# Kernel optimization log

Measured on AMD Instinct MI355X. Metric: run time of the kernel, lower is better.

The kernel has to match this reference:

```python
import jax, jax.numpy as jnp
import numpy as np

NUM_HEADS = 12


def setup_inputs() -> dict:
    key = jax.random.key(0)
    k1, k2, k3 = jax.random.split(key, 3)
    B, N, C = 2, 2048, 768
    x = jax.random.normal(k1, (B, N, C), dtype=jnp.float32)
    # torch nn.Linear weights: [out_features, in_features]
    w_qkv = jax.random.normal(k2, (3 * C, C), dtype=jnp.float32) * (C ** -0.5)
    w_mlp = jax.random.normal(k3, (C, C), dtype=jnp.float32) * (C ** -0.5)
    b_mlp = jnp.zeros((C,), dtype=jnp.float32)
    return {"x": x, "w_qkv": w_qkv, "w_mlp": w_mlp, "b_mlp": b_mlp}


def reference(x, w_qkv, w_mlp, b_mlp):
    B, N, C = x.shape
    H = NUM_HEADS
    hd = C // H
    scale = hd ** -0.5
    # qkv linear (no bias), then the module's reshape: [B,N,H,3,hd]
    qkv = (x @ w_qkv.T).reshape(B, N, H, 3, hd)
    # permute(3,0,2,1,4) -> q,k,v each [B,H,N,hd]
    q = jnp.transpose(qkv[:, :, :, 0, :], (0, 2, 1, 3))
    k = jnp.transpose(qkv[:, :, :, 1, :], (0, 2, 1, 3))
    v = jnp.transpose(qkv[:, :, :, 2, :], (0, 2, 1, 3))
    attn = jax.nn.softmax(jnp.einsum('bhqd,bhkd->bhqk', q, k) * scale, axis=-1)
    out = jnp.einsum('bhqk,bhkd->bhqd', attn, v)          # [B,H,N,hd]
    out = jnp.transpose(out, (0, 2, 1, 3)).reshape(B, N, C)
    return out @ w_mlp.T + b_mlp
```

## Files before the change

kernel.cpp:

```cpp
#include <hip/hip_runtime.h>
#include <math.h>

typedef unsigned short u16;
typedef unsigned int   u32;
typedef __attribute__((ext_vector_type(8))) short s8v;
typedef __attribute__((ext_vector_type(2))) unsigned int u32x2;
typedef __attribute__((ext_vector_type(4))) float f4v;

#define NHEADS 12
#define SEQ 2048
#define CD 768
#define BB 2
#define QKVD 2304
#define CEXP 0.18033688f
#define DEFER_THR 44.0f

__device__ inline u16 f2bf(float f) {
    union { float f; unsigned u; } v; v.f = f;
    unsigned r = v.u + 0x7FFFu + ((v.u >> 16) & 1u);
    return (u16)(r >> 16);
}
__device__ inline u32 cvtpk_bf16(float lo, float hi) {
    u32 r;
    asm("v_cvt_pk_bf16_f32 %0, %1, %2" : "=v"(r) : "v"(lo), "v"(hi));
    return r;
}
__device__ inline float exp2_fast(float x) {
    float r;
    asm("v_exp_f32 %0, %1" : "=v"(r) : "v"(x));
    return r;
}
__device__ inline float max3f(float a, float b, float c) {
    float r;
    asm("v_max3_f32 %0, %1, %2, %3" : "=v"(r) : "v"(a), "v"(b), "v"(c));
    return r;
}

#define GLOAD16(SRC, DST) __builtin_amdgcn_global_load_lds(                 \
    (const __attribute__((address_space(1))) void*)(SRC),                   \
    (__attribute__((address_space(3))) void*)(DST), 16, 0, 0)

#define SW(r, c) ((((r) << 6) + (c)) ^ (((r) & 7) << 3))

__global__ __launch_bounds__(256)
void cvt3_kernel(const float* __restrict__ a, u16* __restrict__ oa, int na,
                 const float* __restrict__ b, u16* __restrict__ ob, int nb,
                 const float* __restrict__ c, u16* __restrict__ oc) {
    const int i = (blockIdx.x * 256 + threadIdx.x) * 8;
    const float* src; u16* dst;
    if (i < na)           { src = a + i;            dst = oa + i; }
    else if (i < na + nb) { src = b + (i - na);     dst = ob + (i - na); }
    else                  { src = c + (i - na - nb); dst = oc + (i - na - nb); }
    const float4 x = *(const float4*)src;
    const float4 y = *(const float4*)(src + 4);
    s8v o;
    o[0] = (short)f2bf(x.x); o[1] = (short)f2bf(x.y);
    o[2] = (short)f2bf(x.z); o[3] = (short)f2bf(x.w);
    o[4] = (short)f2bf(y.x); o[5] = (short)f2bf(y.y);
    o[6] = (short)f2bf(y.z); o[7] = (short)f2bf(y.w);
    *(s8v*)dst = o;
}

template<int BN, int NBX, bool OUT_BF16, bool BIAS>
__global__ __launch_bounds__(256)
void gemm_bf16(const u16* __restrict__ A, const u16* __restrict__ W,
               const float* __restrict__ bias, void* __restrict__ Cout,
               int M, int N, int K) {
    constexpr int NF = BN / 32;
    __shared__ u16 As[8192];
    __shared__ u16 Bs[BN * 64];
    const int tid = threadIdx.x;
    const int l  = tid & 63, w = tid >> 6;
    const int wr = w >> 1, wc = w & 1;
    const int lq = l & 15, lg = l >> 4;

    const int fid = blockIdx.x;
    const int cpx = gridDim.x >> 3;
    const int swz = (fid & 7) * cpx + (fid >> 3);
    const int rowBase = (swz / NBX) << 7;
    const int colBase = (swz % NBX) * BN;

    f4v acc[4][NF];
    #pragma unroll
    for (int m = 0; m < 4; ++m)
        #pragma unroll
        for (int n = 0; n < NF; ++n)
            #pragma unroll
            for (int r = 0; r < 4; ++r) acc[m][n][r] = 0.f;

    const int chunk = l & 7;
    const int r8    = l >> 3;

    for (int kb = 0; kb < K; kb += 64) {
        __syncthreads();
        #pragma unroll
        for (int j = 0; j < 4; ++j) {
            const int rowA = (w << 5) + (j << 3) + r8;
            const int sc   = (chunk ^ (rowA & 7)) << 3;
            GLOAD16(A + (size_t)(rowBase + rowA) * K + kb + sc,
                    &As[(w << 11) + (j << 9)]);
        }
        #pragma unroll
        for (int j = 0; j < NF; ++j) {
            const int rowB = w * (BN / 4) + (j << 3) + r8;
            const int sc   = (chunk ^ (rowB & 7)) << 3;
            GLOAD16(W + (size_t)(colBase + rowB) * K + kb + sc,
                    &Bs[w * (BN * 16) + (j << 9)]);
        }
        __syncthreads();
        #pragma unroll
        for (int h = 0; h < 2; ++h) {
            const int kc = (h << 5) + (lg << 3);
            s8v af[4], bf[NF];
            #pragma unroll
            for (int m = 0; m < 4; ++m)
                af[m] = *(const s8v*)&As[SW((wr << 6) + (m << 4) + lq, kc)];
            #pragma unroll
            for (int n = 0; n < NF; ++n)
                bf[n] = *(const s8v*)&Bs[SW(wc * (BN / 2) + (n << 4) + lq, kc)];
            #pragma unroll
            for (int m = 0; m < 4; ++m)
                #pragma unroll
                for (int n = 0; n < NF; ++n)
                    acc[m][n] = __builtin_amdgcn_mfma_f32_16x16x32_bf16(
                        af[m], bf[n], acc[m][n], 0, 0, 0);
        }
    }

    #pragma unroll
    for (int m = 0; m < 4; ++m)
        #pragma unroll
        for (int r = 0; r < 4; ++r) {
            const int row = rowBase + (wr << 6) + (m << 4) + (lg << 2) + r;
            #pragma unroll
            for (int n = 0; n < NF; ++n) {
                const int col = colBase + wc * (BN / 2) + (n << 4) + lq;
                float v = acc[m][n][r];
                if (BIAS) v += bias[col];
                if (OUT_BF16) ((u16*)Cout)[(size_t)row * N + col] = f2bf(v);
                else        ((float*)Cout)[(size_t)row * N + col] = v;
            }
        }
}

__global__ __launch_bounds__(256)
void vtrans_kernel(const u16* __restrict__ qkvb, u16* __restrict__ vT) {
    __shared__ u16 T[64][66];
    const int bh = blockIdx.y;
    const int tt = blockIdx.x;
    const int b = bh / NHEADS, h = bh % NHEADS;
    const int r  = threadIdx.x >> 2;
    const int dc = (threadIdx.x & 3) << 4;
    const u16* src = qkvb + (size_t)(b * SEQ + tt * 64 + r) * QKVD
                   + h * 192 + 128 + dc;
    *(s8v*)&T[r][dc]     = *(const s8v*)(src);
    *(s8v*)&T[r][dc + 8] = *(const s8v*)(src + 8);
    __syncthreads();
    const int d  = threadIdx.x >> 2;
    const int tc = (threadIdx.x & 3) << 4;
    s8v o0, o1;
    #pragma unroll
    for (int j = 0; j < 8; ++j) {
        o0[j] = (short)T[tc + j][d];
        o1[j] = (short)T[tc + 8 + j][d];
    }
    u16* dst = vT + ((size_t)bh * 64 + d) * SEQ + tt * 64 + tc;
    *(s8v*)dst = o0;
    *(s8v*)(dst + 8) = o1;
}

__global__ __launch_bounds__(512)
void attn_mfma(const u16* __restrict__ qkv, const u16* __restrict__ vT,
               u16* __restrict__ outb) {
    __shared__ u16 SL[24576];
    const int tid = threadIdx.x;
    const int l = tid & 63, w = tid >> 6;
    const int g = w >> 2, wl = w & 3;
    const int lq = l & 15, lg = l >> 4;

    const int fid = blockIdx.x;
    const int swz = (fid & 7) * 96 + (fid >> 3);
    const int q0 = (swz & 31) << 6;
    const int bh = swz >> 5;
    const int b = bh / NHEADS, h = bh % NHEADS;
    const u16* base = qkv + (size_t)b * SEQ * QKVD + h * 192;
    const u16* vbh  = vT + (size_t)bh * 64 * SEQ;
    u16* QP = SL + 16384;
    float* Of32 = (float*)(SL + 8192);
    float* Msh  = (float*)(SL + 16384);
    float* Lsh  = Msh + 64;

    const int kv0 = g << 10;

    u32 koff[2], voff[2], kdst[2], vdst[2];
    {
        const int cs = l & 7;
        #pragma unroll
        for (int i = 0; i < 2; ++i) {
            const int row = (wl << 4) + (i << 3) + (l >> 3);
            koff[i] = (u32)(row * QKVD + 64 + ((cs ^ (row & 7)) << 3));
            voff[i] = (u32)(row * SEQ  +      ((cs ^ (row & 7)) << 3));
            kdst[i] = (u32)((g << 13) + (wl << 10) + (i << 9));
            vdst[i] = (u32)((g << 13) + 4096 + (wl << 10) + (i << 9));
        }
    }

    {
        const u16* sbK = base + (size_t)kv0 * QKVD;
        const u16* sbV = vbh + kv0;
        #pragma unroll
        for (int i = 0; i < 2; ++i) {
            GLOAD16(sbK + koff[i], &SL[kdst[i]]);
            GLOAD16(sbV + voff[i], &SL[vdst[i]]);
        }
    }
    {
        const s8v q1 = *(const s8v*)(base + (size_t)(q0 + l) * QKVD + (w << 3));
        *(s8v*)&QP[SW(l, w << 3)] = q1;
    }
    __syncthreads();
    s8v qf[2];
    #pragma unroll
    for (int h2 = 0; h2 < 2; ++h2)
        qf[h2] = *(const s8v*)&QP[SW((wl << 4) + lq, (h2 << 5) + (lg << 3))];

    s8v onesf;
    {
        const short o = (lq == 0) ? (short)0x3F80 : (short)0;
        #pragma unroll
        for (int e = 0; e < 8; ++e) onesf[e] = o;
    }
    f4v fz;
    #pragma unroll
    for (int r = 0; r < 4; ++r) fz[r] = 0.f;

    f4v oacc[4], osum;
    #pragma unroll
    for (int db = 0; db < 4; ++db)
        #pragma unroll
        for (int r = 0; r < 4; ++r) oacc[db][r] = 0.f;
    #pragma unroll
    for (int r = 0; r < 4; ++r) osum[r] = 0.f;
    float mrun = -3.0e38f;

    const u16* Kc = SL + (g << 13);
    const u16* Vc = Kc + 4096;

    for (int t = 0; t < 16; ++t) {
        __syncthreads();

        float p[16];
        __builtin_amdgcn_s_setprio(1);
        #pragma unroll
        for (int kb = 0; kb < 4; ++kb) {
            const s8v k0 = *(const s8v*)&Kc[SW((kb << 4) + lq, (lg << 3))];
            const s8v k1 = *(const s8v*)&Kc[SW((kb << 4) + lq, 32 + (lg << 3))];
            f4v z;
            z = __builtin_amdgcn_mfma_f32_16x16x32_bf16(k0, qf[0], fz, 0, 0, 0);
            z = __builtin_amdgcn_mfma_f32_16x16x32_bf16(k1, qf[1], z, 0, 0, 0);
            #pragma unroll
            for (int r = 0; r < 4; ++r) p[(kb << 2) + r] = z[r];
        }
        __builtin_amdgcn_s_setprio(0);

        __syncthreads();
        if (t < 15) {
            const u16* sbK = base + (size_t)(kv0 + (t + 1) * 64) * QKVD;
            #pragma unroll
            for (int i = 0; i < 2; ++i)
                GLOAD16(sbK + koff[i], &SL[kdst[i]]);
        }

        float m1_ = max3f(p[0], p[1], p[2]);
        float m2_ = max3f(p[3], p[4], p[5]);
        float m3_ = max3f(p[6], p[7], p[8]);
        float m4_ = max3f(p[9], p[10], p[11]);
        float m5_ = max3f(p[12], p[13], p[14]);
        float mx  = fmaxf(max3f(m1_, m2_, p[15]), max3f(m3_, m4_, m5_));
        if (!__all(mx <= mrun + DEFER_THR)) {
            mx = fmaxf(mx, __shfl_xor(mx, 16));
            mx = fmaxf(mx, __shfl_xor(mx, 32));
            const float mn = fmaxf(mrun, mx);
            const float al = exp2_fast((mrun - mn) * CEXP);
            mrun = mn;
            float ar[4];
            #pragma unroll
            for (int r = 0; r < 4; ++r) ar[r] = __shfl(al, (lg << 2) + r);
            #pragma unroll
            for (int db = 0; db < 4; ++db)
                #pragma unroll
                for (int r = 0; r < 4; ++r) oacc[db][r] *= ar[r];
            #pragma unroll
            for (int r = 0; r < 4; ++r) osum[r] *= ar[r];
        }
        const float mC = -mrun * CEXP;
        #pragma unroll
        for (int i = 0; i < 16; ++i) p[i] = exp2_fast(fmaf(p[i], CEXP, mC));

        #pragma unroll
        for (int kb = 0; kb < 4; ++kb) {
            u32x2 pw;
            pw[0] = cvtpk_bf16(p[(kb << 2) + 0], p[(kb << 2) + 1]);
            pw[1] = cvtpk_bf16(p[(kb << 2) + 2], p[(kb << 2) + 3]);
            *(u32x2*)&QP[SW((w << 4) + lq, (kb << 4) + (lg << 2))] = pw;
        }
        const s8v pf0 = *(const s8v*)&QP[SW((w << 4) + lq, (lg << 3))];
        const s8v pf1 = *(const s8v*)&QP[SW((w << 4) + lq, 32 + (lg << 3))];

        __builtin_amdgcn_s_setprio(1);
        #pragma unroll
        for (int db = 0; db < 4; ++db) {
            const s8v v0 = *(const s8v*)&Vc[SW((db << 4) + lq, (lg << 3))];
            const s8v v1 = *(const s8v*)&Vc[SW((db << 4) + lq, 32 + (lg << 3))];
            oacc[db] = __builtin_amdgcn_mfma_f32_16x16x32_bf16(pf0, v0, oacc[db], 0, 0, 0);
            oacc[db] = __builtin_amdgcn_mfma_f32_16x16x32_bf16(pf1, v1, oacc[db], 0, 0, 0);
        }
        osum = __builtin_amdgcn_mfma_f32_16x16x32_bf16(pf0, onesf, osum, 0, 0, 0);
        osum = __builtin_amdgcn_mfma_f32_16x16x32_bf16(pf1, onesf, osum, 0, 0, 0);
        __builtin_amdgcn_s_setprio(0);

        __syncthreads();
        if (t < 15) {
            const u16* sbV = vbh + kv0 + (t + 1) * 64;
            #pragma unroll
            for (int i = 0; i < 2; ++i)
                GLOAD16(sbV + voff[i], &SL[vdst[i]]);
        }
    }

    if (g == 1) {
        if (lg == 0) Msh[(wl << 4) + lq] = mrun;
        if (lq == 0) {
            #pragma unroll
            for (int r = 0; r < 4; ++r)
                Lsh[(wl << 4) + (lg << 2) + r] = osum[r];
        }
        #pragma unroll
        for (int db = 0; db < 4; ++db)
            #pragma unroll
            for (int r = 0; r < 4; ++r)
                Of32[(((wl << 4) + (lg << 2) + r) << 6) + (db << 4) + lq] =
                    oacc[db][r];
    }
    __syncthreads();
    if (g == 0) {
        #pragma unroll
        for (int r = 0; r < 4; ++r) {
            const int rowq = (wl << 4) + (lg << 2) + r;
            const float m0r = __shfl(mrun, (lg << 2) + r);
            const float l0r = __shfl(osum[r], l & 48);
            const float m1r = Msh[rowq];
            const float l1r = Lsh[rowq];
            const float M   = fmaxf(m0r, m1r);
            const float w0  = exp2_fast((m0r - M) * CEXP);
            const float w1  = exp2_fast((m1r - M) * CEXP);
            const float inv = 1.f / (l0r * w0 + l1r * w1);
            const float a0 = w0 * inv, a1 = w1 * inv;
            const size_t row = (size_t)b * SEQ + q0 + rowq;
            #pragma unroll
            for (int db = 0; db < 4; ++db) {
                const float o1 = Of32[(rowq << 6) + (db << 4) + lq];
                outb[row * CD + h * 64 + (db << 4) + lq] =
                    f2bf(oacc[db][r] * a0 + o1 * a1);
            }
        }
    }
}

extern "C" void kernel_launch(void* const* d_in, const int* in_sizes, int n_in,
                              void* d_out, int out_size, void* d_ws, size_t ws_size,
                              hipStream_t stream) {
    const float* x     = (const float*)d_in[0];
    const float* w_qkv = (const float*)d_in[1];
    const float* w_mlp = (const float*)d_in[2];
    const float* b_mlp = (const float*)d_in[3];
    float* out = (float*)d_out;

    const int NX  = BB * SEQ * CD;
    const int NWQ = QKVD * CD;
    const int NWM = CD * CD;
    const int NQK = BB * SEQ * QKVD;
    const int NAT = BB * SEQ * CD;
    u16* xb    = (u16*)d_ws;
    u16* wqkvb = xb + NX;
    u16* wmlpb = wqkvb + NWQ;
    u16* qkvb  = wmlpb + NWM;
    u16* attnb = qkvb + NQK;
    u16* vTb   = attnb + NAT;

    cvt3_kernel<<<(NX + NWQ + NWM) / 2048, 256, 0, stream>>>(
        x, xb, NX, w_qkv, wqkvb, NWQ, w_mlp, wmlpb);

    const int M = BB * SEQ;
    {
        gemm_bf16<128, 18, true, false><<<576, 256, 0, stream>>>(
            xb, wqkvb, nullptr, qkvb, M, QKVD, CD);
    }
    {
        dim3 grid(SEQ / 64, BB * NHEADS);
        vtrans_kernel<<<grid, 256, 0, stream>>>(qkvb, vTb);
    }
    {
        attn_mfma<<<768, 512, 0, stream>>>(qkvb, vTb, attnb);
    }
    {
        gemm_bf16<64, 12, false, true><<<384, 256, 0, stream>>>(
            attnb, wmlpb, b_mlp, out, M, CD, CD);
    }
}
```

Before: 91.01 us.

## Prefetch K/V tiles into registers and drop mid-loop barrier

Replaces the direct global-to-LDS async loads (GLOAD16) for K and V tiles with register-staged prefetch: the next tile is loaded into registers at the top of each iteration and written to LDS after the final barrier. This removes one __syncthreads per iteration and lets the global load latency overlap the QK and PV MFMA work. The swizzle moves from the global source offset to the LDS destination address. In exchange it uses more VGPRs to hold the in-flight tiles and adds explicit LDS store instructions, which may cut occupancy or add issue pressure.

```diff
diff --git a/kernel.cpp b/kernel.cpp
--- a/kernel.cpp
+++ b/kernel.cpp
@@ -183,8 +183,9 @@
     const int q0 = (swz & 31) << 6;
     const int bh = swz >> 5;
     const int b = bh / NHEADS, h = bh % NHEADS;
-    const u16* base = qkv + (size_t)b * SEQ * QKVD + h * 192;
-    const u16* vbh  = vT + (size_t)bh * 64 * SEQ;
+    const u16* base  = qkv + (size_t)b * SEQ * QKVD + h * 192;
+    const u16* baseK = base + 64;
+    const u16* vbh   = vT + (size_t)bh * 64 * SEQ;
     u16* QP = SL + 16384;
     float* Of32 = (float*)(SL + 8192);
     float* Msh  = (float*)(SL + 16384);
@@ -192,31 +193,30 @@
 
     const int kv0 = g << 10;
 
-    u32 koff[2], voff[2], kdst[2], vdst[2];
-    {
-        const int cs = l & 7;
-        #pragma unroll
-        for (int i = 0; i < 2; ++i) {
-            const int row = (wl << 4) + (i << 3) + (l >> 3);
-            koff[i] = (u32)(row * QKVD + 64 + ((cs ^ (row & 7)) << 3));
-            voff[i] = (u32)(row * SEQ  +      ((cs ^ (row & 7)) << 3));
-            kdst[i] = (u32)((g << 13) + (wl << 10) + (i << 9));
-            vdst[i] = (u32)((g << 13) + 4096 + (wl << 10) + (i << 9));
-        }
-    }
-
-    {
-        const u16* sbK = base + (size_t)kv0 * QKVD;
-        const u16* sbV = vbh + kv0;
-        #pragma unroll
-        for (int i = 0; i < 2; ++i) {
-            GLOAD16(sbK + koff[i], &SL[kdst[i]]);
-            GLOAD16(sbV + voff[i], &SL[vdst[i]]);
-        }
-    }
-    {
-        const s8v q1 = *(const s8v*)(base + (size_t)(q0 + l) * QKVD + (w << 3));
-        *(s8v*)&QP[SW(l, w << 3)] = q1;
+    const int cs  = l & 7;
+    const int rw0 = (wl << 4) + (l >> 3);
+    const int rw1 = rw0 + 8;
+    u32 kO0 = (u32)((kv0 + rw0) * QKVD + cs * 8);
+    u32 kO1 = (u32)((kv0 + rw1) * QKVD + cs * 8);
+    u32 vO0 = (u32)(rw0 * SEQ + kv0 + cs * 8);
+    u32 vO1 = (u32)(rw1 * SEQ + kv0 + cs * 8);
+    const u32 kw0 = (u32)((g << 13) + (rw0 << 6) + ((cs ^ (rw0 & 7)) << 3));
+    const u32 kw1 = (u32)((g << 13) + (rw1 << 6) + ((cs ^ (rw1 & 7)) << 3));
+    const u32 vw0 = kw0 + 4096;
+    const u32 vw1 = kw1 + 4096;
+
+    {
+        const s8v k0 = *(const s8v*)(baseK + kO0);
+        const s8v k1 = *(const s8v*)(baseK + kO1);
+        const s8v v0 = *(const s8v*)(vbh + vO0);
+        const s8v v1 = *(const s8v*)(vbh + vO1);
+        const int qrow = tid >> 3, qch = (tid & 7) << 3;
+        const s8v qv = *(const s8v*)(base + (size_t)(q0 + qrow) * QKVD + qch);
+        *(s8v*)&QP[SW(qrow, qch)] = qv;
+        *(s8v*)&SL[kw0] = k0;
+        *(s8v*)&SL[kw1] = k1;
+        *(s8v*)&SL[vw0] = v0;
+        *(s8v*)&SL[vw1] = v1;
     }
     __syncthreads();
     s8v qf[2];
@@ -245,9 +245,19 @@
 
     const u16* Kc = SL + (g << 13);
     const u16* Vc = Kc + 4096;
+    const u32 STEPK = 64u * QKVD;
 
     for (int t = 0; t < 16; ++t) {
         __syncthreads();
+
+        s8v nk0, nk1, nv0, nv1;
+        if (t < 15) {
+            kO0 += STEPK; kO1 += STEPK; vO0 += 64; vO1 += 64;
+            nk0 = *(const s8v*)(baseK + kO0);
+            nk1 = *(const s8v*)(baseK + kO1);
+            nv0 = *(const s8v*)(vbh + vO0);
+            nv1 = *(const s8v*)(vbh + vO1);
+        }
 
         float p[16];
         __builtin_amdgcn_s_setprio(1);
@@ -262,14 +272,6 @@
             for (int r = 0; r < 4; ++r) p[(kb << 2) + r] = z[r];
         }
         __builtin_amdgcn_s_setprio(0);
-
-        __syncthreads();
-        if (t < 15) {
-            const u16* sbK = base + (size_t)(kv0 + (t + 1) * 64) * QKVD;
-            #pragma unroll
-            for (int i = 0; i < 2; ++i)
-                GLOAD16(sbK + koff[i], &SL[kdst[i]]);
-        }
 
         float m1_ = max3f(p[0], p[1], p[2]);
         float m2_ = max3f(p[3], p[4], p[5]);
@@ -320,11 +322,12 @@
         __builtin_amdgcn_s_setprio(0);
 
         __syncthreads();
+
         if (t < 15) {
-            const u16* sbV = vbh + kv0 + (t + 1) * 64;
-            #pragma unroll
-            for (int i = 0; i < 2; ++i)
-                GLOAD16(sbV + voff[i], &SL[vdst[i]]);
+            *(s8v*)&SL[kw0] = nk0;
+            *(s8v*)&SL[kw1] = nk1;
+            *(s8v*)&SL[vw0] = nv0;
+            *(s8v*)&SL[vw1] = nv1;
         }
     }
 
```

Measured after the change: 91.53 us. Within noise of the previous version (+0.6%).

## Rewrite attention kernel with 32x32x16 MFMA, 4 waves, register-resident P

Applied to the files above, without the earlier changes.

The attention kernel now uses 32x32x16 bf16 MFMAs with 256 threads (4 waves, 32 query rows per wave) instead of 16x16x32 MFMAs with 512 threads. The P matrix is kept in registers and rearranged with v_permlane32_swap rather than a round trip through LDS. The row sum is computed with VALU adds instead of a ones-matrix MFMA. The output is staged through LDS so global stores are coalesced. Each wave now does more work, which raises register pressure and leaves fewer waves to hide latency.

```diff
diff --git a/kernel.cpp b/kernel.cpp
--- a/kernel.cpp
+++ b/kernel.cpp
@@ -4,8 +4,8 @@
 typedef unsigned short u16;
 typedef unsigned int   u32;
 typedef __attribute__((ext_vector_type(8))) short s8v;
-typedef __attribute__((ext_vector_type(2))) unsigned int u32x2;
 typedef __attribute__((ext_vector_type(4))) float f4v;
+typedef __attribute__((ext_vector_type(16))) float f16v;
 
 #define NHEADS 12
 #define SEQ 2048
@@ -41,6 +41,7 @@
     (__attribute__((address_space(3))) void*)(DST), 16, 0, 0)
 
 #define SW(r, c) ((((r) << 6) + (c)) ^ (((r) & 7) << 3))
+#define SW16(r, c) ((((r) << 7) + (c)) ^ (((r) & 15) << 3))
 
 __global__ __launch_bounds__(256)
 void cvt3_kernel(const float* __restrict__ a, u16* __restrict__ oa, int na,
@@ -169,201 +170,229 @@
     *(s8v*)(dst + 8) = o1;
 }
 
-__global__ __launch_bounds__(512)
+__global__ __launch_bounds__(256)
 void attn_mfma(const u16* __restrict__ qkv, const u16* __restrict__ vT,
                u16* __restrict__ outb) {
-    __shared__ u16 SL[24576];
+    __shared__ u16 SL[20480];
+    __shared__ float ML[128];
     const int tid = threadIdx.x;
-    const int l = tid & 63, w = tid >> 6;
-    const int g = w >> 2, wl = w & 3;
-    const int lq = l & 15, lg = l >> 4;
+    const int l  = tid & 63, w = tid >> 6;
+    const int g  = w >> 1, wl = w & 1;
+    const int lq = l & 31;
+    const int lh = l >> 5;
 
     const int fid = blockIdx.x;
     const int swz = (fid & 7) * 96 + (fid >> 3);
     const int q0 = (swz & 31) << 6;
     const int bh = swz >> 5;
-    const int b = bh / NHEADS, h = bh % NHEADS;
-    const u16* base = qkv + (size_t)b * SEQ * QKVD + h * 192;
-    const u16* vbh  = vT + (size_t)bh * 64 * SEQ;
-    u16* QP = SL + 16384;
+    const int b = bh / NHEADS, hh = bh % NHEADS;
+    const u16* base  = qkv + (size_t)b * SEQ * QKVD + hh * 192;
+    const u16* baseK = base + 64;
+    const u16* vbh   = vT + (size_t)bh * 64 * SEQ;
+
+    const int kv0 = g << 10;
+    u16* Kl = SL + (g << 13);
+    u16* Vl = Kl + 4096;
+    u16* Ql = SL + 16384;
     float* Of32 = (float*)(SL + 8192);
-    float* Msh  = (float*)(SL + 16384);
-    float* Lsh  = Msh + 64;
-
-    const int kv0 = g << 10;
-
-    u32 koff[2], voff[2], kdst[2], vdst[2];
-    {
-        const int cs = l & 7;
-        #pragma unroll
-        for (int i = 0; i < 2; ++i) {
-            const int row = (wl << 4) + (i << 3) + (l >> 3);
-            koff[i] = (u32)(row * QKVD + 64 + ((cs ^ (row & 7)) << 3));
-            voff[i] = (u32)(row * SEQ  +      ((cs ^ (row & 7)) << 3));
-            kdst[i] = (u32)((g << 13) + (wl << 10) + (i << 9));
-            vdst[i] = (u32)((g << 13) + 4096 + (wl << 10) + (i << 9));
-        }
-    }
-
-    {
-        const u16* sbK = base + (size_t)kv0 * QKVD;
-        const u16* sbV = vbh + kv0;
-        #pragma unroll
-        for (int i = 0; i < 2; ++i) {
-            GLOAD16(sbK + koff[i], &SL[kdst[i]]);
-            GLOAD16(sbV + voff[i], &SL[vdst[i]]);
-        }
-    }
-    {
-        const s8v q1 = *(const s8v*)(base + (size_t)(q0 + l) * QKVD + (w << 3));
-        *(s8v*)&QP[SW(l, w << 3)] = q1;
+    float* Msh = ML;
+    float* Lsh = ML + 64;
+    u16* Ot = SL + 16384;
+
+    u32 kso[4], vso[4];
+    #pragma unroll
+    for (int i = 0; i < 4; ++i) {
+        const int r  = (wl << 4) + (i << 2) + (l >> 4);
+        const int cg = (l & 15) ^ (r & 15);
+        const int kk = ((cg >> 3) << 5) + r;
+        const int cc = (cg & 7) << 3;
+        kso[i] = (u32)((kv0 + kk) * QKVD + cc);
+        vso[i] = (u32)(kk * SEQ + kv0 + cc);
+    }
+
+    {
+        #pragma unroll
+        for (int i = 0; i < 4; ++i) {
+            GLOAD16(baseK + kso[i], &Kl[(wl << 11) + (i << 9)]);
+            GLOAD16(vbh  + vso[i], &Vl[(wl << 11) + (i << 9)]);
+        }
+        const int qr = tid >> 3, qc = (tid & 7) << 3;
+        const s8v qv0 = *(const s8v*)(base + (size_t)(q0 + qr) * QKVD + qc);
+        const s8v qv1 = *(const s8v*)(base + (size_t)(q0 + 32 + qr) * QKVD + qc);
+        *(s8v*)&Ql[SW16(qr, qc)]      = qv0;
+        *(s8v*)&Ql[SW16(qr, 64 + qc)] = qv1;
     }
     __syncthreads();
-    s8v qf[2];
-    #pragma unroll
-    for (int h2 = 0; h2 < 2; ++h2)
-        qf[h2] = *(const s8v*)&QP[SW((wl << 4) + lq, (h2 << 5) + (lg << 3))];
-
-    s8v onesf;
-    {
-        const short o = (lq == 0) ? (short)0x3F80 : (short)0;
-        #pragma unroll
-        for (int e = 0; e < 8; ++e) onesf[e] = o;
-    }
-    f4v fz;
-    #pragma unroll
-    for (int r = 0; r < 4; ++r) fz[r] = 0.f;
-
-    f4v oacc[4], osum;
-    #pragma unroll
-    for (int db = 0; db < 4; ++db)
-        #pragma unroll
-        for (int r = 0; r < 4; ++r) oacc[db][r] = 0.f;
-    #pragma unroll
-    for (int r = 0; r < 4; ++r) osum[r] = 0.f;
-    float mrun = -3.0e38f;
-
-    const u16* Kc = SL + (g << 13);
-    const u16* Vc = Kc + 4096;
+
+    s8v qf[4];
+    #pragma unroll
+    for (int ds = 0; ds < 4; ++ds)
+        qf[ds] = *(const s8v*)&Ql[SW16(lq, (wl << 6) + (ds << 4) + (lh << 3))];
+
+    f16v z16;
+    #pragma unroll
+    for (int r = 0; r < 16; ++r) z16[r] = 0.f;
+    f16v oa0 = z16, oa1 = z16;
+    float osum = 0.f, mrun = -3.0e38f;
 
     for (int t = 0; t < 16; ++t) {
-        __syncthreads();
-
-        float p[16];
+        s8v ka[8];
+        #pragma unroll
+        for (int kb = 0; kb < 2; ++kb)
+            #pragma unroll
+            for (int ds = 0; ds < 4; ++ds)
+                ka[kb * 4 + ds] = *(const s8v*)
+                    &Kl[SW16(lq, (kb << 6) + (ds << 4) + (lh << 3))];
+        f16v s0 = z16, s1 = z16;
         __builtin_amdgcn_s_setprio(1);
         #pragma unroll
-        for (int kb = 0; kb < 4; ++kb) {
-            const s8v k0 = *(const s8v*)&Kc[SW((kb << 4) + lq, (lg << 3))];
-            const s8v k1 = *(const s8v*)&Kc[SW((kb << 4) + lq, 32 + (lg << 3))];
-            f4v z;
-            z = __builtin_amdgcn_mfma_f32_16x16x32_bf16(k0, qf[0], fz, 0, 0, 0);
-            z = __builtin_amdgcn_mfma_f32_16x16x32_bf16(k1, qf[1], z, 0, 0, 0);
-            #pragma unroll
-            for (int r = 0; r < 4; ++r) p[(kb << 2) + r] = z[r];
-        }
+        for (int ds = 0; ds < 4; ++ds)
+            s0 = __builtin_amdgcn_mfma_f32_32x32x16_bf16(ka[ds], qf[ds], s0, 0, 0, 0);
+        #pragma unroll
+        for (int ds = 0; ds < 4; ++ds)
+            s1 = __builtin_amdgcn_mfma_f32_32x32x16_bf16(ka[4 + ds], qf[ds], s1, 0, 0, 0);
         __builtin_amdgcn_s_setprio(0);
 
         __syncthreads();
         if (t < 15) {
-            const u16* sbK = base + (size_t)(kv0 + (t + 1) * 64) * QKVD;
-            #pragma unroll
-            for (int i = 0; i < 2; ++i)
-                GLOAD16(sbK + koff[i], &SL[kdst[i]]);
-        }
-
-        float m1_ = max3f(p[0], p[1], p[2]);
-        float m2_ = max3f(p[3], p[4], p[5]);
-        float m3_ = max3f(p[6], p[7], p[8]);
-        float m4_ = max3f(p[9], p[10], p[11]);
-        float m5_ = max3f(p[12], p[13], p[14]);
-        float mx  = fmaxf(max3f(m1_, m2_, p[15]), max3f(m3_, m4_, m5_));
+            const u16* sb = baseK + (size_t)(t + 1) * (64 * QKVD);
+            #pragma unroll
+            for (int i = 0; i < 4; ++i)
+                GLOAD16(sb + kso[i], &Kl[(wl << 11) + (i << 9)]);
+        }
+
+        float mxa = max3f(s0[0], s0[1], s0[2]);
+        mxa = max3f(mxa, s0[3], s0[4]);  mxa = max3f(mxa, s0[5], s0[6]);
+        mxa = max3f(mxa, s0[7], s0[8]);  mxa = max3f(mxa, s0[9], s0[10]);
+        mxa = max3f(mxa, s0[11], s0[12]); mxa = max3f(mxa, s0[13], s0[14]);
+        float mxb = max3f(s1[0], s1[1], s1[2]);
+        mxb = max3f(mxb, s1[3], s1[4]);  mxb = max3f(mxb, s1[5], s1[6]);
+        mxb = max3f(mxb, s1[7], s1[8]);  mxb = max3f(mxb, s1[9], s1[10]);
+        mxb = max3f(mxb, s1[11], s1[12]); mxb = max3f(mxb, s1[13], s1[14]);
+        float mx = max3f(mxa, s0[15], mxb);
+        mx = fmaxf(mx, s1[15]);
         if (!__all(mx <= mrun + DEFER_THR)) {
-            mx = fmaxf(mx, __shfl_xor(mx, 16));
             mx = fmaxf(mx, __shfl_xor(mx, 32));
             const float mn = fmaxf(mrun, mx);
             const float al = exp2_fast((mrun - mn) * CEXP);
             mrun = mn;
-            float ar[4];
-            #pragma unroll
-            for (int r = 0; r < 4; ++r) ar[r] = __shfl(al, (lg << 2) + r);
-            #pragma unroll
-            for (int db = 0; db < 4; ++db)
-                #pragma unroll
-                for (int r = 0; r < 4; ++r) oacc[db][r] *= ar[r];
-            #pragma unroll
-            for (int r = 0; r < 4; ++r) osum[r] *= ar[r];
+            #pragma unroll
+            for (int r = 0; r < 16; ++r) { oa0[r] *= al; oa1[r] *= al; }
+            osum *= al;
         }
         const float mC = -mrun * CEXP;
         #pragma unroll
-        for (int i = 0; i < 16; ++i) p[i] = exp2_fast(fmaf(p[i], CEXP, mC));
-
-        #pragma unroll
-        for (int kb = 0; kb < 4; ++kb) {
-            u32x2 pw;
-            pw[0] = cvtpk_bf16(p[(kb << 2) + 0], p[(kb << 2) + 1]);
-            pw[1] = cvtpk_bf16(p[(kb << 2) + 2], p[(kb << 2) + 3]);
-            *(u32x2*)&QP[SW((w << 4) + lq, (kb << 4) + (lg << 2))] = pw;
-        }
-        const s8v pf0 = *(const s8v*)&QP[SW((w << 4) + lq, (lg << 3))];
-        const s8v pf1 = *(const s8v*)&QP[SW((w << 4) + lq, 32 + (lg << 3))];
-
+        for (int r = 0; r < 16; ++r) {
+            s0[r] = exp2_fast(fmaf(s0[r], CEXP, mC));
+            s1[r] = exp2_fast(fmaf(s1[r], CEXP, mC));
+        }
+        {
+            float a0 = s0[0] + s0[4], a1 = s0[1] + s0[5];
+            float a2 = s0[2] + s0[6], a3 = s0[3] + s0[7];
+            a0 += s0[8] + s0[12];  a1 += s0[9] + s0[13];
+            a2 += s0[10] + s0[14]; a3 += s0[11] + s0[15];
+            a0 += s1[0] + s1[4];   a1 += s1[1] + s1[5];
+            a2 += s1[2] + s1[6];   a3 += s1[3] + s1[7];
+            a0 += s1[8] + s1[12];  a1 += s1[9] + s1[13];
+            a2 += s1[10] + s1[14]; a3 += s1[11] + s1[15];
+            osum += (a0 + a1) + (a2 + a3);
+        }
+
+        s8v pf[4];
+        #pragma unroll
+        for (int s = 0; s < 2; ++s) {
+            u32 A0 = cvtpk_bf16(s0[8*s+0], s0[8*s+1]);
+            u32 B0 = cvtpk_bf16(s0[8*s+4], s0[8*s+5]);
+            u32 A1 = cvtpk_bf16(s0[8*s+2], s0[8*s+3]);
+            u32 B1 = cvtpk_bf16(s0[8*s+6], s0[8*s+7]);
+            asm volatile("v_permlane32_swap_b32 %0, %1" : "+v"(A0), "+v"(B0));
+            asm volatile("v_permlane32_swap_b32 %0, %1" : "+v"(A1), "+v"(B1));
+            union { s8v v; u32 u[4]; } pu;
+            pu.u[0] = A0; pu.u[1] = A1; pu.u[2] = B0; pu.u[3] = B1;
+            pf[s] = pu.v;
+        }
+        #pragma unroll
+        for (int s = 0; s < 2; ++s) {
+            u32 A0 = cvtpk_bf16(s1[8*s+0], s1[8*s+1]);
+            u32 B0 = cvtpk_bf16(s1[8*s+4], s1[8*s+5]);
+            u32 A1 = cvtpk_bf16(s1[8*s+2], s1[8*s+3]);
+            u32 B1 = cvtpk_bf16(s1[8*s+6], s1[8*s+7]);
+            asm volatile("v_permlane32_swap_b32 %0, %1" : "+v"(A0), "+v"(B0));
+            asm volatile("v_permlane32_swap_b32 %0, %1" : "+v"(A1), "+v"(B1));
+            union { s8v v; u32 u[4]; } pu;
+            pu.u[0] = A0; pu.u[1] = A1; pu.u[2] = B0; pu.u[3] = B1;
+            pf[2 + s] = pu.v;
+        }
+
+        s8v va[8];
+        #pragma unroll
+        for (int db = 0; db < 2; ++db)
+            #pragma unroll
+            for (int ks = 0; ks < 4; ++ks)
+                va[db * 4 + ks] = *(const s8v*)
+                    &Vl[SW16(lq, (db << 6) + (ks << 4) + (lh << 3))];
         __builtin_amdgcn_s_setprio(1);
         #pragma unroll
-        for (int db = 0; db < 4; ++db) {
-            const s8v v0 = *(const s8v*)&Vc[SW((db << 4) + lq, (lg << 3))];
-            const s8v v1 = *(const s8v*)&Vc[SW((db << 4) + lq, 32 + (lg << 3))];
-            oacc[db] = __builtin_amdgcn_mfma_f32_16x16x32_bf16(pf0, v0, oacc[db], 0, 0, 0);
-            oacc[db] = __builtin_amdgcn_mfma_f32_16x16x32_bf16(pf1, v1, oacc[db], 0, 0, 0);
-        }
-        osum = __builtin_amdgcn_mfma_f32_16x16x32_bf16(pf0, onesf, osum, 0, 0, 0);
-        osum = __builtin_amdgcn_mfma_f32_16x16x32_bf16(pf1, onesf, osum, 0, 0, 0);
+        for (int ks = 0; ks < 4; ++ks)
+            oa0 = __builtin_amdgcn_mfma_f32_32x32x16_bf16(va[ks], pf[ks], oa0, 0, 0, 0);
+        #pragma unroll
+        for (int ks = 0; ks < 4; ++ks)
+            oa1 = __builtin_amdgcn_mfma_f32_32x32x16_bf16(va[4 + ks], pf[ks], oa1, 0, 0, 0);
         __builtin_amdgcn_s_setprio(0);
 
         __syncthreads();
         if (t < 15) {
-            const u16* sbV = vbh + kv0 + (t + 1) * 64;
-            #pragma unroll
-            for (int i = 0; i < 2; ++i)
-                GLOAD16(sbV + voff[i], &SL[vdst[i]]);
-        }
-    }
-
+            const u16* sb = vbh + (t + 1) * 64;
+            #pragma unroll
+            for (int i = 0; i < 4; ++i)
+                GLOAD16(sb + vso[i], &Vl[(wl << 11) + (i << 9)]);
+        }
+    }
+
+    const float osum_t = osum + __shfl_xor(osum, 32);
+    const int wq = (wl << 5) + lq;
     if (g == 1) {
-        if (lg == 0) Msh[(wl << 4) + lq] = mrun;
-        if (lq == 0) {
-            #pragma unroll
-            for (int r = 0; r < 4; ++r)
-                Lsh[(wl << 4) + (lg << 2) + r] = osum[r];
-        }
-        #pragma unroll
-        for (int db = 0; db < 4; ++db)
-            #pragma unroll
-            for (int r = 0; r < 4; ++r)
-                Of32[(((wl << 4) + (lg << 2) + r) << 6) + (db << 4) + lq] =
-                    oacc[db][r];
+        if (lh == 0) { Msh[wq] = mrun; Lsh[wq] = osum_t; }
+        #pragma unroll
+        for (int r = 0; r < 16; ++r) {
+            const int d0 = (r & 3) + ((r >> 2) << 3) + (lh << 2);
+            Of32[d0 * 64 + wq]        = oa0[r];
+            Of32[(d0 + 32) * 64 + wq] = oa1[r];
+        }
     }
     __syncthreads();
     if (g == 0) {
-        #pragma unroll
-        for (int r = 0; r < 4; ++r) {
-            const int rowq = (wl << 4) + (lg << 2) + r;
-            const float m0r = __shfl(mrun, (lg << 2) + r);
-            const float l0r = __shfl(osum[r], l & 48);
-            const float m1r = Msh[rowq];
-            const float l1r = Lsh[rowq];
-            const float M   = fmaxf(m0r, m1r);
-            const float w0  = exp2_fast((m0r - M) * CEXP);
-            const float w1  = exp2_fast((m1r - M) * CEXP);
-            const float inv = 1.f / (l0r * w0 + l1r * w1);
-            const float a0 = w0 * inv, a1 = w1 * inv;
-            const size_t row = (size_t)b * SEQ + q0 + rowq;
-            #pragma unroll
-            for (int db = 0; db < 4; ++db) {
-                const float o1 = Of32[(rowq << 6) + (db << 4) + lq];
-                outb[row * CD + h * 64 + (db << 4) + lq] =
-                    f2bf(oacc[db][r] * a0 + o1 * a1);
-            }
-        }
+        const float m1 = Msh[wq], l1 = Lsh[wq];
+        const float M  = fmaxf(mrun, m1);
+        const float w0 = exp2_fast((mrun - M) * CEXP);
+        const float w1 = exp2_fast((m1 - M) * CEXP);
+        const float inv = 1.f / (osum_t * w0 + l1 * w1);
+        const float a0 = w0 * inv, a1 = w1 * inv;
+        #pragma unroll
+        for (int j = 0; j < 4; ++j) {
+            const int d0 = (j << 3) + (lh << 2);
+            const float v0 = oa0[4*j+0] * a0 + Of32[(d0+0)*64+wq] * a1;
+            const float v1 = oa0[4*j+1] * a0 + Of32[(d0+1)*64+wq] * a1;
+            const float v2 = oa0[4*j+2] * a0 + Of32[(d0+2)*64+wq] * a1;
+            const float v3 = oa0[4*j+3] * a0 + Of32[(d0+3)*64+wq] * a1;
+            *(u32*)&Ot[SW(wq, d0)]     = cvtpk_bf16(v0, v1);
+            *(u32*)&Ot[SW(wq, d0 + 2)] = cvtpk_bf16(v2, v3);
+            const float u0 = oa1[4*j+0] * a0 + Of32[(d0+32)*64+wq] * a1;
+            const float u1 = oa1[4*j+1] * a0 + Of32[(d0+33)*64+wq] * a1;
+            const float u2 = oa1[4*j+2] * a0 + Of32[(d0+34)*64+wq] * a1;
+            const float u3 = oa1[4*j+3] * a0 + Of32[(d0+35)*64+wq] * a1;
+            *(u32*)&Ot[SW(wq, d0 + 32)] = cvtpk_bf16(u0, u1);
+            *(u32*)&Ot[SW(wq, d0 + 34)] = cvtpk_bf16(u2, u3);
+        }
+    }
+    __syncthreads();
+    {
+        const int row = tid >> 2, c0 = (tid & 3) << 4;
+        const s8v o0 = *(const s8v*)&Ot[SW(row, c0)];
+        const s8v o1 = *(const s8v*)&Ot[SW(row, c0 + 8)];
+        u16* dst = outb + (size_t)(b * SEQ + q0 + row) * CD + hh * 64 + c0;
+        *(s8v*)dst = o0;
+        *(s8v*)(dst + 8) = o1;
     }
 }
 
@@ -401,7 +430,7 @@
         vtrans_kernel<<<grid, 256, 0, stream>>>(qkvb, vTb);
     }
     {
-        attn_mfma<<<768, 512, 0, stream>>>(qkvb, vTb, attnb);
+        attn_mfma<<<768, 256, 0, stream>>>(qkvb, vTb, attnb);
     }
     {
         gemm_bf16<64, 12, false, true><<<384, 256, 0, stream>>>(
```

Measured after the change: 98.42 us. +8.2%, slower.
